# Performance work log

Hardware: AMD Instinct MI355X
Metric: run time of the kernel (lower is better)

## Reference

```python
import jax, jax.numpy as jnp
import numpy as np

HEADS = 8
DIM_HEAD = 64
DIM = 512
NUM_BANDS = 32
MAX_FREQ = 32.0
NORM_SCALE = 10.0
RPE_DIM = (NUM_BANDS * 2 + 1) * 2  # 130


def setup_inputs() -> dict:
    key = jax.random.key(0)
    ks = jax.random.split(key, 9)
    B, N = 2, 512
    inner = HEADS * DIM_HEAD
    h2 = HEADS * 2
    inp = {
        "x": jax.random.normal(ks[0], (B, N, DIM), dtype=jnp.float32),
        "positions": jax.random.uniform(ks[1], (B, N, 2), dtype=jnp.float32),
        "W_qkv": jax.random.normal(ks[2], (DIM, 3 * inner), dtype=jnp.float32) / np.sqrt(DIM),
        "W_out": jax.random.normal(ks[3], (inner, DIM), dtype=jnp.float32) / np.sqrt(inner),
        "b_out": jnp.zeros((DIM,), dtype=jnp.float32),
        "rpe_W1": jax.random.normal(ks[4], (RPE_DIM, h2), dtype=jnp.float32) / np.sqrt(RPE_DIM),
        "rpe_b1": jnp.zeros((h2,), dtype=jnp.float32),
        "rpe_W2": jax.random.normal(ks[5], (h2, HEADS), dtype=jnp.float32) / np.sqrt(h2),
        "rpe_b2": jnp.zeros((HEADS,), dtype=jnp.float32),
    }
    return inp


def _fourier_encode(x):
    # x: [...], returns [..., 2*NUM_BANDS+1]
    freqs = jnp.linspace(1.0, MAX_FREQ, NUM_BANDS, dtype=x.dtype)
    angles = x[..., None] * freqs * jnp.pi
    return jnp.concatenate([x[..., None], jnp.sin(angles), jnp.cos(angles)], axis=-1)


def _rpe_bias(positions, W1, b1, W2, b2):
    # positions: [B, N, 2] -> bias [B, H, N, N]
    delta = positions[:, None, :, :] - positions[:, :, None, :]  # key_pos_j - query_pos_i
    dx = delta[..., 0] / NORM_SCALE
    dy = delta[..., 1] / NORM_SCALE
    dx = dx / (1.0 + jnp.abs(dx))
    dy = dy / (1.0 + jnp.abs(dy))
    feats = jnp.concatenate([_fourier_encode(dx), _fourier_encode(dy)], axis=-1)  # [B,N,N,130]
    h = jax.nn.gelu(feats @ W1 + b1, approximate=False)
    bias = h @ W2 + b2  # [B, N, N, H]
    return jnp.transpose(bias, (0, 3, 1, 2))  # [B, H, N, N]


def reference(x, positions, W_qkv, W_out, b_out, rpe_W1, rpe_b1, rpe_W2, rpe_b2):
    B, N, _ = x.shape
    H, d = HEADS, DIM_HEAD
    scale = d ** (-0.5)
    qkv = x @ W_qkv  # [B, N, 3*H*d]
    q, k, v = jnp.split(qkv, 3, axis=-1)
    q = q.reshape(B, N, H, d)
    k = k.reshape(B, N, H, d)
    v = v.reshape(B, N, H, d)
    scores = jnp.einsum('bihd,bjhd->bhij', q, k) * scale
    scores = scores + _rpe_bias(positions, rpe_W1, rpe_b1, rpe_W2, rpe_b2)
    attn = jax.nn.softmax(scores, axis=-1)
    out = jnp.einsum('bhij,bjhd->bihd', attn, v).reshape(B, N, H * d)
    return out @ W_out + b_out
```

## Files before the change

### kernel.cpp

```cpp
#include <hip/hip_runtime.h>
#include <hip/hip_fp16.h>
#include <math.h>

typedef __attribute__((ext_vector_type(8))) _Float16 f16x8;
typedef __attribute__((ext_vector_type(4))) float f32x4;

#define TBL 512
#define UMAXV (1.0f/11.0f)

__device__ __forceinline__ int swq(int row, int q) {
  return row * 64 + ((q ^ (row & 7)) << 3);
}
__device__ __forceinline__ f16x8 cvt8(float4 a, float4 b) {
  f16x8 r;
  r[0] = (_Float16)a.x; r[1] = (_Float16)a.y;
  r[2] = (_Float16)a.z; r[3] = (_Float16)a.w;
  r[4] = (_Float16)b.x; r[5] = (_Float16)b.y;
  r[6] = (_Float16)b.z; r[7] = (_Float16)b.w;
  return r;
}

__global__ __launch_bounds__(256) void k_prep(
    const float* __restrict__ Wqkv, const float* __restrict__ Wout,
    const float* __restrict__ W1, const float* __restrict__ b1,
    _Float16* __restrict__ Wt, _Float16* __restrict__ Wot,
    __half* __restrict__ Tx, __half* __restrict__ Ty) {
  __shared__ float Tt[32 * 33];
  const int t = threadIdx.x;
  const int bid = blockIdx.x;
  if (bid >= 1024) {
    int gid = (bid - 1024) * 256 + t;
    int e = gid >> 5, c = gid & 31;
    float u = -UMAXV + (2.0f * UMAXV) * (float)e / (float)(TBL - 1);
    const int xpart = (c < 16);
    const int col = c & 15;
    const int base = xpart ? 0 : 65;
    float sum = u * W1[base * 16 + col] + (xpart ? b1[col] : 0.0f);
    float s1, c1;
    sincosf(u * 3.14159265358979323846f, &s1, &c1);
    float sk = s1, ck = c1;
    for (int k = 1; k <= 32; ++k) {
      sum += sk * W1[(base + k) * 16 + col] + ck * W1[(base + 32 + k) * 16 + col];
      float ns = sk * c1 + ck * s1;
      ck = ck * c1 - sk * s1;
      sk = ns;
    }
    (xpart ? Tx : Ty)[e * 16 + col] = __float2half(sum);
    return;
  }
  int k0, n0, ncols;
  const float* W;
  _Float16* O;
  if (bid < 768) {
    k0 = (bid / 48) * 32; n0 = (bid % 48) * 32; ncols = 1536;
    W = Wqkv; O = Wt;
  } else {
    int tile = bid - 768;
    k0 = (tile / 16) * 32; n0 = (tile % 16) * 32; ncols = 512;
    W = Wout; O = Wot;
  }
  {
    int kl = t >> 3, nl = (t & 7) * 4;
    float4 v = *(const float4*)&W[(k0 + kl) * ncols + n0 + nl];
    Tt[kl * 33 + nl + 0] = v.x;
    Tt[kl * 33 + nl + 1] = v.y;
    Tt[kl * 33 + nl + 2] = v.z;
    Tt[kl * 33 + nl + 3] = v.w;
  }
  __syncthreads();
  {
    int nl = t >> 3, kq = (t & 7) * 4;
    ushort4 h;
    h.x = __builtin_bit_cast(unsigned short, (_Float16)Tt[(kq + 0) * 33 + nl]);
    h.y = __builtin_bit_cast(unsigned short, (_Float16)Tt[(kq + 1) * 33 + nl]);
    h.z = __builtin_bit_cast(unsigned short, (_Float16)Tt[(kq + 2) * 33 + nl]);
    h.w = __builtin_bit_cast(unsigned short, (_Float16)Tt[(kq + 3) * 33 + nl]);
    *(ushort4*)&O[(n0 + nl) * 512 + k0 + kq] = h;
  }
}

__global__ __launch_bounds__(512) void k_fused(
    const float* __restrict__ x, const _Float16* __restrict__ Wt,
    _Float16* __restrict__ q16, _Float16* __restrict__ k16,
    _Float16* __restrict__ vt16,
    const float* __restrict__ pos,
    const __half* __restrict__ Tx, const __half* __restrict__ Ty,
    const float* __restrict__ W2, const float* __restrict__ b2,
    _Float16* __restrict__ bias) {
  __shared__ __align__(16) unsigned short SM[16384];
  const int bid = blockIdx.x;
  const int t = threadIdx.x;

  if (bid < 192) {
    _Float16* Ah = (_Float16*)SM;
    _Float16* Bh = (_Float16*)SM + 8192;
    const int mt = bid / 24, nt = bid % 24;
    const int m0 = mt * 128, n0 = nt * 64;
    const int w = t >> 6, lane = t & 63, blk = lane >> 4, jc = lane & 15;
    const int mw = (w & 3) * 32, nw = (w >> 2) * 32;
    const int sa = t >> 3, sq = t & 7;

    f32x4 acc[2][2];
    #pragma unroll
    for (int i = 0; i < 2; ++i)
      #pragma unroll
      for (int j = 0; j < 2; ++j) acc[i][j] = f32x4{0.f, 0.f, 0.f, 0.f};

    float4 pax[2][2];
    f16x8 pbv;
    #pragma unroll
    for (int c = 0; c < 2; ++c) {
      const float* xp = &x[(m0 + sa + c * 64) * 512 + sq * 8];
      pax[c][0] = *(const float4*)xp;
      pax[c][1] = *(const float4*)(xp + 4);
    }
    pbv = *(const f16x8*)&Wt[(n0 + sa) * 512 + sq * 8];

    for (int it = 0; it < 8; ++it) {
      #pragma unroll
      for (int c = 0; c < 2; ++c)
        *(f16x8*)&Ah[swq(sa + c * 64, sq)] = cvt8(pax[c][0], pax[c][1]);
      *(f16x8*)&Bh[swq(sa, sq)] = pbv;
      __syncthreads();
      if (it < 7) {
        int k0 = (it + 1) * 64;
        #pragma unroll
        for (int c = 0; c < 2; ++c) {
          const float* xp = &x[(m0 + sa + c * 64) * 512 + k0 + sq * 8];
          pax[c][0] = *(const float4*)xp;
          pax[c][1] = *(const float4*)(xp + 4);
        }
        pbv = *(const f16x8*)&Wt[(n0 + sa) * 512 + k0 + sq * 8];
      }
      #pragma unroll
      for (int h = 0; h < 2; ++h) {
        int q = h * 4 + blk;
        f16x8 a0 = *(const f16x8*)&Ah[swq(mw + jc, q)];
        f16x8 a1 = *(const f16x8*)&Ah[swq(mw + 16 + jc, q)];
        f16x8 b0 = *(const f16x8*)&Bh[swq(nw + jc, q)];
        f16x8 b1 = *(const f16x8*)&Bh[swq(nw + 16 + jc, q)];
        acc[0][0] = __builtin_amdgcn_mfma_f32_16x16x32_f16(a0, b0, acc[0][0], 0, 0, 0);
        acc[0][1] = __builtin_amdgcn_mfma_f32_16x16x32_f16(a0, b1, acc[0][1], 0, 0, 0);
        acc[1][0] = __builtin_amdgcn_mfma_f32_16x16x32_f16(a1, b0, acc[1][0], 0, 0, 0);
        acc[1][1] = __builtin_amdgcn_mfma_f32_16x16x32_f16(a1, b1, acc[1][1], 0, 0, 0);
      }
      __syncthreads();
    }
    const int sec = n0 >> 9;
    const int hh_ = (n0 >> 6) & 7;
    if (sec < 2) {
      _Float16* dst = (sec == 0) ? q16 : k16;
      const float scl = (sec == 0) ? 0.125f : 1.0f;
      #pragma unroll
      for (int i = 0; i < 2; ++i)
        #pragma unroll
        for (int j = 0; j < 2; ++j)
          #pragma unroll
          for (int r = 0; r < 4; ++r) {
            int tok = m0 + mw + i * 16 + blk * 4 + r;
            int b = tok >> 9, nn = tok & 511;
            int d = nw + j * 16 + jc;
            dst[((b * 8 + hh_) * 512 + nn) * 64 + d] = (_Float16)(acc[i][j][r] * scl);
          }
    } else {
      _Float16* T = (_Float16*)SM;
      #pragma unroll
      for (int i = 0; i < 2; ++i)
        #pragma unroll
        for (int j = 0; j < 2; ++j)
          #pragma unroll
          for (int r = 0; r < 4; ++r)
            T[(nw + j * 16 + jc) * 136 + mw + i * 16 + blk * 4 + r] =
                (_Float16)acc[i][j][r];
      __syncthreads();
      const int d = t >> 3, tq = t & 7;
      const int b = m0 >> 9, nb = m0 & 511;
      #pragma unroll
      for (int c = 0; c < 2; ++c) {
        int qd = tq + c * 8;
        f16x8 vv = *(const f16x8*)&T[d * 136 + qd * 8];
        *(f16x8*)&vt16[((b * 8 + hh_) * 64 + d) * 512 + nb + qd * 8] = vv;
      }
    }
    return;
  }

  const int gid = (bid - 192) * 512 + t;
  const int b = gid >> 18;
  const int i = (gid >> 9) & 511;
  const int j = gid & 511;
  const float pix = pos[(b * 512 + i) * 2 + 0];
  const float piy = pos[(b * 512 + i) * 2 + 1];
  const float pjx = pos[(b * 512 + j) * 2 + 0];
  const float pjy = pos[(b * 512 + j) * 2 + 1];
  float txv = (pjx - pix) * 0.1f; float ux = txv / (1.0f + fabsf(txv));
  float tyv = (pjy - piy) * 0.1f; float uy = tyv / (1.0f + fabsf(tyv));
  const float invstep = (float)(TBL - 1) / (2.0f * UMAXV);
  float fx = (ux + UMAXV) * invstep;
  int ix = (int)fx; ix = min(max(ix, 0), TBL - 2);
  float wx = fx - (float)ix;
  float fy = (uy + UMAXV) * invstep;
  int iy = (int)fy; iy = min(max(iy, 0), TBL - 2);
  float wy = fy - (float)iy;

  __half hx0[16], hx1[16], hy0[16], hy1[16];
  *(uint4*)&hx0[0] = *(const uint4*)&Tx[ix * 16];
  *(uint4*)&hx0[8] = *(const uint4*)&Tx[ix * 16 + 8];
  *(uint4*)&hx1[0] = *(const uint4*)&Tx[(ix + 1) * 16];
  *(uint4*)&hx1[8] = *(const uint4*)&Tx[(ix + 1) * 16 + 8];
  *(uint4*)&hy0[0] = *(const uint4*)&Ty[iy * 16];
  *(uint4*)&hy0[8] = *(const uint4*)&Ty[iy * 16 + 8];
  *(uint4*)&hy1[0] = *(const uint4*)&Ty[(iy + 1) * 16];
  *(uint4*)&hy1[8] = *(const uint4*)&Ty[(iy + 1) * 16 + 8];

  float o[8];
  #pragma unroll
  for (int c = 0; c < 8; ++c) o[c] = b2[c];
  #pragma unroll
  for (int r = 0; r < 16; ++r) {
    float ax = __half2float(hx0[r]);
    float bx = __half2float(hx1[r]);
    float ay = __half2float(hy0[r]);
    float by = __half2float(hy1[r]);
    float hv = fmaf(wx, bx - ax, ax) + fmaf(wy, by - ay, ay);
    float z = hv * 0.70710678118654752f;
    float az = fabsf(z);
    float tt = __builtin_amdgcn_rcpf(fmaf(0.3275911f, az, 1.0f));
    float poly = ((((1.061405429f * tt - 1.453152027f) * tt + 1.421413741f) * tt
                   - 0.284496736f) * tt + 0.254829592f) * tt;
    float ex = __expf(-z * z);
    float erfv = copysignf(fmaf(-poly, ex, 1.0f), z);
    float g = 0.5f * hv * (1.0f + erfv);
    #pragma unroll
    for (int c = 0; c < 8; ++c)
      o[c] = fmaf(g, W2[r * 8 + c], o[c]);
  }
  #pragma unroll
  for (int c = 0; c < 8; ++c)
    bias[((size_t)(b * 8 + c) * 512 + i) * 512 + j] = (_Float16)o[c];
}

__global__ __launch_bounds__(512) void k_attn(
    const _Float16* __restrict__ q16, const _Float16* __restrict__ k16,
    const _Float16* __restrict__ vt16, const _Float16* __restrict__ bias,
    _Float16* __restrict__ ao16) {
  __shared__ __align__(16) _Float16 psu[8 * 512];
  __shared__ __align__(16) float olds[8 * 16 * 65];
  __shared__ float mls[8 * 16 * 2];
  _Float16* bst = (_Float16*)olds;

  const int bid = blockIdx.x;
  const int it = bid & 31, h = (bid >> 5) & 7, b = bid >> 8;
  const int i0 = it * 16;
  const int bh = b * 8 + h;
  const int tid = threadIdx.x;
  const int w = tid >> 6, lane = tid & 63;
  const int blk = lane >> 4, jc = lane & 15;

  {
    const _Float16* bgp = bias + ((size_t)(bh * 512 + i0)) * 512;
    int brow = tid >> 5, bc = (tid & 31) * 16;
    *(f16x8*)&bst[brow * 520 + bc]     = *(const f16x8*)&bgp[brow * 512 + bc];
    *(f16x8*)&bst[brow * 520 + bc + 8] = *(const f16x8*)&bgp[brow * 512 + bc + 8];
  }

  const int qoff = (bh * 512 + i0 + jc) * 64 + blk * 8;
  const f16x8 qa0 = *(const f16x8*)&q16[qoff];
  const f16x8 qa1 = *(const f16x8*)&q16[qoff + 32];

  float m[4] = {-1e30f, -1e30f, -1e30f, -1e30f};
  float l[4] = {0.f, 0.f, 0.f, 0.f};
  f32x4 o[4];
  #pragma unroll
  for (int dt = 0; dt < 4; ++dt) o[dt] = f32x4{0.f, 0.f, 0.f, 0.f};

  _Float16* pw = &psu[w * 512];
  __syncthreads();

  #pragma unroll
  for (int jt = 0; jt < 2; ++jt) {
    const int j0 = w * 64 + jt * 32;
    const int rA = (bh * 512 + j0 + jc) * 64 + blk * 8;
    const int rB = rA + 16 * 64;
    f16x8 kA0 = *(const f16x8*)&k16[rA];
    f16x8 kA1 = *(const f16x8*)&k16[rA + 32];
    f16x8 kB0 = *(const f16x8*)&k16[rB];
    f16x8 kB1 = *(const f16x8*)&k16[rB + 32];

    f32x4 aA = {0.f, 0.f, 0.f, 0.f};
    aA = __builtin_amdgcn_mfma_f32_16x16x32_f16(qa0, kA0, aA, 0, 0, 0);
    aA = __builtin_amdgcn_mfma_f32_16x16x32_f16(qa1, kA1, aA, 0, 0, 0);
    f32x4 aB = {0.f, 0.f, 0.f, 0.f};
    aB = __builtin_amdgcn_mfma_f32_16x16x32_f16(qa0, kB0, aB, 0, 0, 0);
    aB = __builtin_amdgcn_mfma_f32_16x16x32_f16(qa1, kB1, aB, 0, 0, 0);

    float sA[4], sB[4], sc[4];
    #pragma unroll
    for (int r = 0; r < 4; ++r) {
      const int br = (blk * 4 + r) * 520;
      sA[r] = aA[r] + (float)bst[br + j0 + jc];
      sB[r] = aB[r] + (float)bst[br + j0 + 16 + jc];
    }
    #pragma unroll
    for (int r = 0; r < 4; ++r) {
      float mx = fmaxf(sA[r], sB[r]);
      mx = fmaxf(mx, __shfl_xor(mx, 1, 64));
      mx = fmaxf(mx, __shfl_xor(mx, 2, 64));
      mx = fmaxf(mx, __shfl_xor(mx, 4, 64));
      mx = fmaxf(mx, __shfl_xor(mx, 8, 64));
      float mn = fmaxf(m[r], mx);
      sc[r] = __expf(m[r] - mn);
      m[r] = mn;
      float pA = __expf(sA[r] - mn);
      float pB = __expf(sB[r] - mn);
      float ps = pA + pB;
      ps += __shfl_xor(ps, 1, 64);
      ps += __shfl_xor(ps, 2, 64);
      ps += __shfl_xor(ps, 4, 64);
      ps += __shfl_xor(ps, 8, 64);
      l[r] = l[r] * sc[r] + ps;
      pw[(blk * 4 + r) * 32 + jc] = (_Float16)pA;
      pw[(blk * 4 + r) * 32 + 16 + jc] = (_Float16)pB;
    }
    #pragma unroll
    for (int dt = 0; dt < 4; ++dt)
      #pragma unroll
      for (int r = 0; r < 4; ++r)
        o[dt][r] *= sc[r];
    f16x8 pf = *(const f16x8*)&pw[jc * 32 + blk * 8];
    #pragma unroll
    for (int dt = 0; dt < 4; ++dt) {
      const int va = (bh * 64 + dt * 16 + jc) * 512 + j0 + blk * 8;
      f16x8 vh = *(const f16x8*)&vt16[va];
      o[dt] = __builtin_amdgcn_mfma_f32_16x16x32_f16(pf, vh, o[dt], 0, 0, 0);
    }
  }
  __syncthreads();
  #pragma unroll
  for (int dt = 0; dt < 4; ++dt)
    #pragma unroll
    for (int r = 0; r < 4; ++r)
      olds[(w * 16 + blk * 4 + r) * 65 + dt * 16 + jc] = o[dt][r];
  if (jc == 0) {
    #pragma unroll
    for (int r = 0; r < 4; ++r) {
      mls[(w * 16 + blk * 4 + r) * 2 + 0] = m[r];
      mls[(w * 16 + blk * 4 + r) * 2 + 1] = l[r];
    }
  }
  __syncthreads();
  #pragma unroll
  for (int itx = 0; itx < 2; ++itx) {
    int idx = tid + itx * 512;
    int q = idx >> 6, d = idx & 63;
    float M = -1e30f;
    #pragma unroll
    for (int ww = 0; ww < 8; ++ww) M = fmaxf(M, mls[(ww * 16 + q) * 2]);
    float L = 0.f, acc = 0.f;
    #pragma unroll
    for (int ww = 0; ww < 8; ++ww) {
      float e = __expf(mls[(ww * 16 + q) * 2] - M);
      L += mls[(ww * 16 + q) * 2 + 1] * e;
      acc += olds[(ww * 16 + q) * 65 + d] * e;
    }
    ao16[(b * 512 + i0 + q) * 512 + h * 64 + d] = (_Float16)(acc / L);
  }
}

__global__ __launch_bounds__(256) void k_out(
    const _Float16* __restrict__ ao16, const _Float16* __restrict__ Wot,
    const float* __restrict__ bout, float* __restrict__ out) {
  __shared__ __align__(16) unsigned short SM[6144];
  _Float16* Ah = (_Float16*)SM;
  _Float16* Bh = (_Float16*)SM + 2048;

  const int bid = blockIdx.x;
  const int mt = bid >> 3, nt = bid & 7;
  const int m0 = mt * 32, n0 = nt * 64;
  const int t = threadIdx.x;
  const int w = t >> 6, lane = t & 63, blk = lane >> 4, jc = lane & 15;
  const int mh_ = (w & 1) * 16, nh_ = (w >> 1) * 32;
  const int sm = t >> 3, sq = t & 7;

  f32x4 acc[2];
  acc[0] = f32x4{0.f, 0.f, 0.f, 0.f};
  acc[1] = f32x4{0.f, 0.f, 0.f, 0.f};

  f16x8 pa, pb[2];
  {
    pa = *(const f16x8*)&ao16[(m0 + sm) * 512 + sq * 8];
    #pragma unroll
    for (int c = 0; c < 2; ++c)
      pb[c] = *(const f16x8*)&Wot[(n0 + sm + c * 32) * 512 + sq * 8];
  }
  for (int it = 0; it < 8; ++it) {
    *(f16x8*)&Ah[swq(sm, sq)] = pa;
    #pragma unroll
    for (int c = 0; c < 2; ++c)
      *(f16x8*)&Bh[swq(sm + c * 32, sq)] = pb[c];
    __syncthreads();
    if (it < 7) {
      int k0 = (it + 1) * 64;
      pa = *(const f16x8*)&ao16[(m0 + sm) * 512 + k0 + sq * 8];
      #pragma unroll
      for (int c = 0; c < 2; ++c)
        pb[c] = *(const f16x8*)&Wot[(n0 + sm + c * 32) * 512 + k0 + sq * 8];
    }
    #pragma unroll
    for (int h = 0; h < 2; ++h) {
      int q = h * 4 + blk;
      f16x8 a0 = *(const f16x8*)&Ah[swq(mh_ + jc, q)];
      f16x8 b0 = *(const f16x8*)&Bh[swq(nh_ + jc, q)];
      f16x8 b1 = *(const f16x8*)&Bh[swq(nh_ + 16 + jc, q)];
      acc[0] = __builtin_amdgcn_mfma_f32_16x16x32_f16(a0, b0, acc[0], 0, 0, 0);
      acc[1] = __builtin_amdgcn_mfma_f32_16x16x32_f16(a0, b1, acc[1], 0, 0, 0);
    }
    __syncthreads();
  }
  #pragma unroll
  for (int j = 0; j < 2; ++j) {
    int n = n0 + nh_ + j * 16 + jc;
    float bb = bout[n];
    #pragma unroll
    for (int r = 0; r < 4; ++r) {
      int row = m0 + mh_ + blk * 4 + r;
      out[row * 512 + n] = acc[j][r] + bb;
    }
  }
}

extern "C" void kernel_launch(void* const* d_in, const int* in_sizes, int n_in,
                              void* d_out, int out_size, void* d_ws, size_t ws_size,
                              hipStream_t stream) {
  const float* x    = (const float*)d_in[0];
  const float* pos  = (const float*)d_in[1];
  const float* Wqkv = (const float*)d_in[2];
  const float* Wout = (const float*)d_in[3];
  const float* bout = (const float*)d_in[4];
  const float* W1   = (const float*)d_in[5];
  const float* b1   = (const float*)d_in[6];
  const float* W2   = (const float*)d_in[7];
  const float* b2   = (const float*)d_in[8];
  float* out = (float*)d_out;
  char* base = (char*)d_ws;

  __half* Tx       = (__half*)(base);
  __half* Ty       = (__half*)(base + 16384);
  _Float16* Wt     = (_Float16*)(base + 32768);
  _Float16* Wot    = (_Float16*)(base + 1605632);
  _Float16* q16    = (_Float16*)(base + 2129920);
  _Float16* k16    = (_Float16*)(base + 3178496);
  _Float16* vt16   = (_Float16*)(base + 4227072);
  _Float16* bias16 = (_Float16*)(base + 5275648);
  _Float16* ao16   = (_Float16*)(base + 13664256);

  hipLaunchKernelGGL(k_prep, dim3(1088), dim3(256), 0, stream,
                     Wqkv, Wout, W1, b1, Wt, Wot, Tx, Ty);
  hipLaunchKernelGGL(k_fused, dim3(1216), dim3(512), 0, stream,
                     x, Wt, q16, k16, vt16, pos, Tx, Ty, W2, b2, bias16);
  hipLaunchKernelGGL(k_attn, dim3(512), dim3(512), 0, stream,
                     q16, k16, vt16, bias16, ao16);
  hipLaunchKernelGGL(k_out, dim3(256), dim3(256), 0, stream,
                     ao16, Wot, bout, out);
}
```

Measured before the change: 43.97 us.

## Merge all stages into one persistent cooperative kernel with grid syncs

Replaces four separate kernel launches (weight prep, QKV/bias, attention, output projection) with a single cooperative kernel of 256 blocks. The blocks loop over the former work items and separate the stages with grid-wide barriers. This removes launch overhead and inter-kernel gaps. In exchange, each stage is limited to 256 resident blocks with 512 threads, which lowers parallelism for the bias and prep stages, and the output GEMM tile shape changes to 64x64 over 128 blocks.

```diff
diff --git a/kernel.cpp b/kernel.cpp
--- a/kernel.cpp
+++ b/kernel.cpp
@@ -1,6 +1,9 @@
 #include <hip/hip_runtime.h>
 #include <hip/hip_fp16.h>
+#include <hip/hip_cooperative_groups.h>
 #include <math.h>
+
+namespace cg = cooperative_groups;
 
 typedef __attribute__((ext_vector_type(8))) _Float16 f16x8;
 typedef __attribute__((ext_vector_type(4))) float f32x4;
@@ -20,16 +23,31 @@
   return r;
 }
 
-__global__ __launch_bounds__(256) void k_prep(
+__global__ __launch_bounds__(512) void k_all(
+    const float* __restrict__ x, const float* __restrict__ pos,
     const float* __restrict__ Wqkv, const float* __restrict__ Wout,
-    const float* __restrict__ W1, const float* __restrict__ b1,
-    _Float16* __restrict__ Wt, _Float16* __restrict__ Wot,
-    __half* __restrict__ Tx, __half* __restrict__ Ty) {
-  __shared__ float Tt[32 * 33];
+    const float* __restrict__ bout, const float* __restrict__ W1,
+    const float* __restrict__ b1, const float* __restrict__ W2,
+    const float* __restrict__ b2, float* __restrict__ out,
+    char* __restrict__ ws) {
+  __shared__ __align__(16) char SMEM[42496];
+
+  __half*   Tx     = (__half*)(ws);
+  __half*   Ty     = (__half*)(ws + 16384);
+  _Float16* Wt     = (_Float16*)(ws + 32768);
+  _Float16* Wot    = (_Float16*)(ws + 1605632);
+  _Float16* q16    = (_Float16*)(ws + 2129920);
+  _Float16* k16    = (_Float16*)(ws + 3178496);
+  _Float16* vt16   = (_Float16*)(ws + 4227072);
+  _Float16* bias16 = (_Float16*)(ws + 5275648);
+  _Float16* ao16   = (_Float16*)(ws + 13664256);
+
+  cg::grid_group grid = cg::this_grid();
+  const int bid = blockIdx.x;
   const int t = threadIdx.x;
-  const int bid = blockIdx.x;
-  if (bid >= 1024) {
-    int gid = (bid - 1024) * 256 + t;
+
+  if (bid >= 224) {
+    int gid = (bid - 224) * 512 + t;
     int e = gid >> 5, c = gid & 31;
     float u = -UMAXV + (2.0f * UMAXV) * (float)e / (float)(TBL - 1);
     const int xpart = (c < 16);
@@ -46,385 +64,367 @@
       sk = ns;
     }
     (xpart ? Tx : Ty)[e * 16 + col] = __float2half(sum);
-    return;
+  } else {
+    const int sub = t >> 8, tl = t & 255;
+    float* Tt = (float*)SMEM + sub * (32 * 33);
+    for (int u = bid; u < 512; u += 224) {
+      int tile = u * 2 + sub;
+      int k0, n0, ncols;
+      const float* W;
+      _Float16* O;
+      if (tile < 768) {
+        k0 = (tile / 48) * 32; n0 = (tile % 48) * 32; ncols = 1536;
+        W = Wqkv; O = Wt;
+      } else {
+        int q = tile - 768;
+        k0 = (q / 16) * 32; n0 = (q % 16) * 32; ncols = 512;
+        W = Wout; O = Wot;
+      }
+      {
+        int kl = tl >> 3, nl = (tl & 7) * 4;
+        float4 v = *(const float4*)&W[(k0 + kl) * ncols + n0 + nl];
+        Tt[kl * 33 + nl + 0] = v.x;
+        Tt[kl * 33 + nl + 1] = v.y;
+        Tt[kl * 33 + nl + 2] = v.z;
+        Tt[kl * 33 + nl + 3] = v.w;
+      }
+      __syncthreads();
+      {
+        int nl = tl >> 3, kq = (tl & 7) * 4;
+        ushort4 h;
+        h.x = __builtin_bit_cast(unsigned short, (_Float16)Tt[(kq + 0) * 33 + nl]);
+        h.y = __builtin_bit_cast(unsigned short, (_Float16)Tt[(kq + 1) * 33 + nl]);
+        h.z = __builtin_bit_cast(unsigned short, (_Float16)Tt[(kq + 2) * 33 + nl]);
+        h.w = __builtin_bit_cast(unsigned short, (_Float16)Tt[(kq + 3) * 33 + nl]);
+        *(ushort4*)&O[(n0 + nl) * 512 + k0 + kq] = h;
+      }
+      __syncthreads();
+    }
   }
-  int k0, n0, ncols;
-  const float* W;
-  _Float16* O;
-  if (bid < 768) {
-    k0 = (bid / 48) * 32; n0 = (bid % 48) * 32; ncols = 1536;
-    W = Wqkv; O = Wt;
-  } else {
-    int tile = bid - 768;
-    k0 = (tile / 16) * 32; n0 = (tile % 16) * 32; ncols = 512;
-    W = Wout; O = Wot;
+  grid.sync();
+
+  for (int u = bid; u < 1216; u += 256) {
+    if (u < 192) {
+      _Float16* Ah = (_Float16*)SMEM;
+      _Float16* Bh = (_Float16*)SMEM + 8192;
+      const int mt = u / 24, nt = u % 24;
+      const int m0 = mt * 128, n0 = nt * 64;
+      const int w = t >> 6, lane = t & 63, blk = lane >> 4, jc = lane & 15;
+      const int mw = (w & 3) * 32, nw = (w >> 2) * 32;
+      const int sa = t >> 3, sq = t & 7;
+
+      f32x4 acc[2][2];
+      #pragma unroll
+      for (int i = 0; i < 2; ++i)
+        #pragma unroll
+        for (int j = 0; j < 2; ++j) acc[i][j] = f32x4{0.f, 0.f, 0.f, 0.f};
+
+      float4 pax[2][2];
+      f16x8 pbv;
+      #pragma unroll
+      for (int c = 0; c < 2; ++c) {
+        const float* xp = &x[(m0 + sa + c * 64) * 512 + sq * 8];
+        pax[c][0] = *(const float4*)xp;
+        pax[c][1] = *(const float4*)(xp + 4);
+      }
+      pbv = *(const f16x8*)&Wt[(n0 + sa) * 512 + sq * 8];
+
+      for (int it = 0; it < 8; ++it) {
+        #pragma unroll
+        for (int c = 0; c < 2; ++c)
+          *(f16x8*)&Ah[swq(sa + c * 64, sq)] = cvt8(pax[c][0], pax[c][1]);
+        *(f16x8*)&Bh[swq(sa, sq)] = pbv;
+        __syncthreads();
+        if (it < 7) {
+          int k0 = (it + 1) * 64;
+          #pragma unroll
+          for (int c = 0; c < 2; ++c) {
+            const float* xp = &x[(m0 + sa + c * 64) * 512 + k0 + sq * 8];
+            pax[c][0] = *(const float4*)xp;
+            pax[c][1] = *(const float4*)(xp + 4);
+          }
+          pbv = *(const f16x8*)&Wt[(n0 + sa) * 512 + k0 + sq * 8];
+        }
+        #pragma unroll
+        for (int h = 0; h < 2; ++h) {
+          int q = h * 4 + blk;
+          f16x8 a0 = *(const f16x8*)&Ah[swq(mw + jc, q)];
+          f16x8 a1 = *(const f16x8*)&Ah[swq(mw + 16 + jc, q)];
+          f16x8 b0 = *(const f16x8*)&Bh[swq(nw + jc, q)];
+          f16x8 b1 = *(const f16x8*)&Bh[swq(nw + 16 + jc, q)];
+          acc[0][0] = __builtin_amdgcn_mfma_f32_16x16x32_f16(a0, b0, acc[0][0], 0, 0, 0);
+          acc[0][1] = __builtin_amdgcn_mfma_f32_16x16x32_f16(a0, b1, acc[0][1], 0, 0, 0);
+          acc[1][0] = __builtin_amdgcn_mfma_f32_16x16x32_f16(a1, b0, acc[1][0], 0, 0, 0);
+          acc[1][1] = __builtin_amdgcn_mfma_f32_16x16x32_f16(a1, b1, acc[1][1], 0, 0, 0);
+        }
+        __syncthreads();
+      }
+      const int sec = n0 >> 9;
+      const int hh_ = (n0 >> 6) & 7;
+      if (sec < 2) {
+        _Float16* dst = (sec == 0) ? q16 : k16;
+        const float scl = (sec == 0) ? 0.125f : 1.0f;
+        #pragma unroll
+        for (int i = 0; i < 2; ++i)
+          #pragma unroll
+          for (int j = 0; j < 2; ++j)
+            #pragma unroll
+            for (int r = 0; r < 4; ++r) {
+              int tok = m0 + mw + i * 16 + blk * 4 + r;
+              int b = tok >> 9, nn = tok & 511;
+              int d = nw + j * 16 + jc;
+              dst[((b * 8 + hh_) * 512 + nn) * 64 + d] = (_Float16)(acc[i][j][r] * scl);
+            }
+      } else {
+        _Float16* T = (_Float16*)SMEM;
+        #pragma unroll
+        for (int i = 0; i < 2; ++i)
+          #pragma unroll
+          for (int j = 0; j < 2; ++j)
+            #pragma unroll
+            for (int r = 0; r < 4; ++r)
+              T[(nw + j * 16 + jc) * 136 + mw + i * 16 + blk * 4 + r] =
+                  (_Float16)acc[i][j][r];
+        __syncthreads();
+        const int d = t >> 3, tq = t & 7;
+        const int b = m0 >> 9, nb = m0 & 511;
+        #pragma unroll
+        for (int c = 0; c < 2; ++c) {
+          int qd = tq + c * 8;
+          f16x8 vv = *(const f16x8*)&T[d * 136 + qd * 8];
+          *(f16x8*)&vt16[((b * 8 + hh_) * 64 + d) * 512 + nb + qd * 8] = vv;
+        }
+        __syncthreads();
+      }
+    } else {
+      const int gid = (u - 192) * 512 + t;
+      const int b = gid >> 18;
+      const int i = (gid >> 9) & 511;
+      const int j = gid & 511;
+      const float pix = pos[(b * 512 + i) * 2 + 0];
+      const float piy = pos[(b * 512 + i) * 2 + 1];
+      const float pjx = pos[(b * 512 + j) * 2 + 0];
+      const float pjy = pos[(b * 512 + j) * 2 + 1];
+      float txv = (pjx - pix) * 0.1f; float ux = txv / (1.0f + fabsf(txv));
+      float tyv = (pjy - piy) * 0.1f; float uy = tyv / (1.0f + fabsf(tyv));
+      const float invstep = (float)(TBL - 1) / (2.0f * UMAXV);
+      float fx = (ux + UMAXV) * invstep;
+      int ix = (int)fx; ix = min(max(ix, 0), TBL - 2);
+      float wx = fx - (float)ix;
+      float fy = (uy + UMAXV) * invstep;
+      int iy = (int)fy; iy = min(max(iy, 0), TBL - 2);
+      float wy = fy - (float)iy;
+
+      __half hx0[16], hx1[16], hy0[16], hy1[16];
+      *(uint4*)&hx0[0] = *(const uint4*)&Tx[ix * 16];
+      *(uint4*)&hx0[8] = *(const uint4*)&Tx[ix * 16 + 8];
+      *(uint4*)&hx1[0] = *(const uint4*)&Tx[(ix + 1) * 16];
+      *(uint4*)&hx1[8] = *(const uint4*)&Tx[(ix + 1) * 16 + 8];
+      *(uint4*)&hy0[0] = *(const uint4*)&Ty[iy * 16];
+      *(uint4*)&hy0[8] = *(const uint4*)&Ty[iy * 16 + 8];
+      *(uint4*)&hy1[0] = *(const uint4*)&Ty[(iy + 1) * 16];
+      *(uint4*)&hy1[8] = *(const uint4*)&Ty[(iy + 1) * 16 + 8];
+
+      float o[8];
+      #pragma unroll
+      for (int c = 0; c < 8; ++c) o[c] = b2[c];
+      #pragma unroll
+      for (int r = 0; r < 16; ++r) {
+        float ax = __half2float(hx0[r]);
+        float bx = __half2float(hx1[r]);
+        float ay = __half2float(hy0[r]);
+        float by = __half2float(hy1[r]);
+        float hv = fmaf(wx, bx - ax, ax) + fmaf(wy, by - ay, ay);
+        float z = hv * 0.70710678118654752f;
+        float az = fabsf(z);
+        float tt = __builtin_amdgcn_rcpf(fmaf(0.3275911f, az, 1.0f));
+        float poly = ((((1.061405429f * tt - 1.453152027f) * tt + 1.421413741f) * tt
+                       - 0.284496736f) * tt + 0.254829592f) * tt;
+        float ex = __expf(-z * z);
+        float erfv = copysignf(fmaf(-poly, ex, 1.0f), z);
+        float g = 0.5f * hv * (1.0f + erfv);
+        #pragma unroll
+        for (int c = 0; c < 8; ++c)
+          o[c] = fmaf(g, W2[r * 8 + c], o[c]);
+      }
+      #pragma unroll
+      for (int c = 0; c < 8; ++c)
+        bias16[((size_t)(b * 8 + c) * 512 + i) * 512 + j] = (_Float16)o[c];
+    }
   }
+  grid.sync();
+
   {
-    int kl = t >> 3, nl = (t & 7) * 4;
-    float4 v = *(const float4*)&W[(k0 + kl) * ncols + n0 + nl];
-    Tt[kl * 33 + nl + 0] = v.x;
-    Tt[kl * 33 + nl + 1] = v.y;
-    Tt[kl * 33 + nl + 2] = v.z;
-    Tt[kl * 33 + nl + 3] = v.w;
+    _Float16* psu = (_Float16*)SMEM;
+    float* olds   = (float*)(SMEM + 8192);
+    float* mls    = (float*)(SMEM + 8192 + 33280);
+    _Float16* bst = (_Float16*)olds;
+
+    for (int u = bid; u < 512; u += 256) {
+      const int itile = u & 31, h = (u >> 5) & 7, b = u >> 8;
+      const int i0 = itile * 16;
+      const int bh = b * 8 + h;
+      const int w = t >> 6, lane = t & 63;
+      const int blk = lane >> 4, jc = lane & 15;
+
+      {
+        const _Float16* bgp = bias16 + ((size_t)(bh * 512 + i0)) * 512;
+        int brow = t >> 5, bc = (t & 31) * 16;
+        *(f16x8*)&bst[brow * 520 + bc]     = *(const f16x8*)&bgp[brow * 512 + bc];
+        *(f16x8*)&bst[brow * 520 + bc + 8] = *(const f16x8*)&bgp[brow * 512 + bc + 8];
+      }
+
+      const int qoff = (bh * 512 + i0 + jc) * 64 + blk * 8;
+      const f16x8 qa0 = *(const f16x8*)&q16[qoff];
+      const f16x8 qa1 = *(const f16x8*)&q16[qoff + 32];
+
+      float m[4] = {-1e30f, -1e30f, -1e30f, -1e30f};
+      float l[4] = {0.f, 0.f, 0.f, 0.f};
+      f32x4 o[4];
+      #pragma unroll
+      for (int dt = 0; dt < 4; ++dt) o[dt] = f32x4{0.f, 0.f, 0.f, 0.f};
+
+      _Float16* pw = &psu[w * 512];
+      __syncthreads();
+
+      #pragma unroll
+      for (int jt = 0; jt < 2; ++jt) {
+        const int j0 = w * 64 + jt * 32;
+        const int rA = (bh * 512 + j0 + jc) * 64 + blk * 8;
+        const int rB = rA + 16 * 64;
+        f16x8 kA0 = *(const f16x8*)&k16[rA];
+        f16x8 kA1 = *(const f16x8*)&k16[rA + 32];
+        f16x8 kB0 = *(const f16x8*)&k16[rB];
+        f16x8 kB1 = *(const f16x8*)&k16[rB + 32];
+
+        f32x4 aA = {0.f, 0.f, 0.f, 0.f};
+        aA = __builtin_amdgcn_mfma_f32_16x16x32_f16(qa0, kA0, aA, 0, 0, 0);
+        aA = __builtin_amdgcn_mfma_f32_16x16x32_f16(qa1, kA1, aA, 0, 0, 0);
+        f32x4 aB = {0.f, 0.f, 0.f, 0.f};
+        aB = __builtin_amdgcn_mfma_f32_16x16x32_f16(qa0, kB0, aB, 0, 0, 0);
+        aB = __builtin_amdgcn_mfma_f32_16x16x32_f16(qa1, kB1, aB, 0, 0, 0);
+
+        float sA[4], sB[4], sc[4];
+        #pragma unroll
+        for (int r = 0; r < 4; ++r) {
+          const int br = (blk * 4 + r) * 520;
+          sA[r] = aA[r] + (float)bst[br + j0 + jc];
+          sB[r] = aB[r] + (float)bst[br + j0 + 16 + jc];
+        }
+        #pragma unroll
+        for (int r = 0; r < 4; ++r) {
+          float mx = fmaxf(sA[r], sB[r]);
+          mx = fmaxf(mx, __shfl_xor(mx, 1, 64));
+          mx = fmaxf(mx, __shfl_xor(mx, 2, 64));
+          mx = fmaxf(mx, __shfl_xor(mx, 4, 64));
+          mx = fmaxf(mx, __shfl_xor(mx, 8, 64));
+          float mn = fmaxf(m[r], mx);
+          sc[r] = __expf(m[r] - mn);
+          m[r] = mn;
+          float pA = __expf(sA[r] - mn);
+          float pB = __expf(sB[r] - mn);
+          float ps = pA + pB;
+          ps += __shfl_xor(ps, 1, 64);
+          ps += __shfl_xor(ps, 2, 64);
+          ps += __shfl_xor(ps, 4, 64);
+          ps += __shfl_xor(ps, 8, 64);
+          l[r] = l[r] * sc[r] + ps;
+          pw[(blk * 4 + r) * 32 + jc] = (_Float16)pA;
+          pw[(blk * 4 + r) * 32 + 16 + jc] = (_Float16)pB;
+        }
+        #pragma unroll
+        for (int dt = 0; dt < 4; ++dt)
+          #pragma unroll
+          for (int r = 0; r < 4; ++r)
+            o[dt][r] *= sc[r];
+        f16x8 pf = *(const f16x8*)&pw[jc * 32 + blk * 8];
+        #pragma unroll
+        for (int dt = 0; dt < 4; ++dt) {
+          const int va = (bh * 64 + dt * 16 + jc) * 512 + j0 + blk * 8;
+          f16x8 vh = *(const f16x8*)&vt16[va];
+          o[dt] = __builtin_amdgcn_mfma_f32_16x16x32_f16(pf, vh, o[dt], 0, 0, 0);
+        }
+      }
+      __syncthreads();
+      #pragma unroll
+      for (int dt = 0; dt < 4; ++dt)
+        #pragma unroll
+        for (int r = 0; r < 4; ++r)
+          olds[(w * 16 + blk * 4 + r) * 65 + dt * 16 + jc] = o[dt][r];
+      if (jc == 0) {
+        #pragma unroll
+        for (int r = 0; r < 4; ++r) {
+          mls[(w * 16 + blk * 4 + r) * 2 + 0] = m[r];
+          mls[(w * 16 + blk * 4 + r) * 2 + 1] = l[r];
+        }
+      }
+      __syncthreads();
+      #pragma unroll
+      for (int itx = 0; itx < 2; ++itx) {
+        int idx = t + itx * 512;
+        int q = idx >> 6, d = idx & 63;
+        float M = -1e30f;
+        #pragma unroll
+        for (int ww = 0; ww < 8; ++ww) M = fmaxf(M, mls[(ww * 16 + q) * 2]);
+        float L = 0.f, acc = 0.f;
+        #pragma unroll
+        for (int ww = 0; ww < 8; ++ww) {
+          float e = __expf(mls[(ww * 16 + q) * 2] - M);
+          L += mls[(ww * 16 + q) * 2 + 1] * e;
+          acc += olds[(ww * 16 + q) * 65 + d] * e;
+        }
+        ao16[(b * 512 + i0 + q) * 512 + h * 64 + d] = (_Float16)(acc / L);
+      }
+      __syncthreads();
+    }
   }
-  __syncthreads();
-  {
-    int nl = t >> 3, kq = (t & 7) * 4;
-    ushort4 h;
-    h.x = __builtin_bit_cast(unsigned short, (_Float16)Tt[(kq + 0) * 33 + nl]);
-    h.y = __builtin_bit_cast(unsigned short, (_Float16)Tt[(kq + 1) * 33 + nl]);
-    h.z = __builtin_bit_cast(unsigned short, (_Float16)Tt[(kq + 2) * 33 + nl]);
-    h.w = __builtin_bit_cast(unsigned short, (_Float16)Tt[(kq + 3) * 33 + nl]);
-    *(ushort4*)&O[(n0 + nl) * 512 + k0 + kq] = h;
-  }
-}
-
-__global__ __launch_bounds__(512) void k_fused(
-    const float* __restrict__ x, const _Float16* __restrict__ Wt,
-    _Float16* __restrict__ q16, _Float16* __restrict__ k16,
-    _Float16* __restrict__ vt16,
-    const float* __restrict__ pos,
-    const __half* __restrict__ Tx, const __half* __restrict__ Ty,
-    const float* __restrict__ W2, const float* __restrict__ b2,
-    _Float16* __restrict__ bias) {
-  __shared__ __align__(16) unsigned short SM[16384];
-  const int bid = blockIdx.x;
-  const int t = threadIdx.x;
-
-  if (bid < 192) {
-    _Float16* Ah = (_Float16*)SM;
-    _Float16* Bh = (_Float16*)SM + 8192;
-    const int mt = bid / 24, nt = bid % 24;
-    const int m0 = mt * 128, n0 = nt * 64;
+  grid.sync();
+
+  if (bid < 128) {
+    _Float16* Ah = (_Float16*)SMEM;
+    _Float16* Bh = (_Float16*)SMEM + 4096;
+    const int mt = bid >> 3, nt = bid & 7;
+    const int m0 = mt * 64, n0 = nt * 64;
     const int w = t >> 6, lane = t & 63, blk = lane >> 4, jc = lane & 15;
-    const int mw = (w & 3) * 32, nw = (w >> 2) * 32;
+    const int mw = (w & 3) * 16, nw = (w >> 2) * 32;
     const int sa = t >> 3, sq = t & 7;
 
-    f32x4 acc[2][2];
-    #pragma unroll
-    for (int i = 0; i < 2; ++i)
-      #pragma unroll
-      for (int j = 0; j < 2; ++j) acc[i][j] = f32x4{0.f, 0.f, 0.f, 0.f};
-
-    float4 pax[2][2];
-    f16x8 pbv;
-    #pragma unroll
-    for (int c = 0; c < 2; ++c) {
-      const float* xp = &x[(m0 + sa + c * 64) * 512 + sq * 8];
-      pax[c][0] = *(const float4*)xp;
-      pax[c][1] = *(const float4*)(xp + 4);
-    }
-    pbv = *(const f16x8*)&Wt[(n0 + sa) * 512 + sq * 8];
+    f32x4 acc[2];
+    acc[0] = f32x4{0.f, 0.f, 0.f, 0.f};
+    acc[1] = f32x4{0.f, 0.f, 0.f, 0.f};
+
+    f16x8 pa = *(const f16x8*)&ao16[(m0 + sa) * 512 + sq * 8];
+    f16x8 pb = *(const f16x8*)&Wot[(n0 + sa) * 512 + sq * 8];
 
     for (int it = 0; it < 8; ++it) {
-      #pragma unroll
-      for (int c = 0; c < 2; ++c)
-        *(f16x8*)&Ah[swq(sa + c * 64, sq)] = cvt8(pax[c][0], pax[c][1]);
-      *(f16x8*)&Bh[swq(sa, sq)] = pbv;
+      *(f16x8*)&Ah[swq(sa, sq)] = pa;
+      *(f16x8*)&Bh[swq(sa, sq)] = pb;
       __syncthreads();
       if (it < 7) {
         int k0 = (it + 1) * 64;
-        #pragma unroll
-        for (int c = 0; c < 2; ++c) {
-          const float* xp = &x[(m0 + sa + c * 64) * 512 + k0 + sq * 8];
-          pax[c][0] = *(const float4*)xp;
-          pax[c][1] = *(const float4*)(xp + 4);
-        }
-        pbv = *(const f16x8*)&Wt[(n0 + sa) * 512 + k0 + sq * 8];
+        pa = *(const f16x8*)&ao16[(m0 + sa) * 512 + k0 + sq * 8];
+        pb = *(const f16x8*)&Wot[(n0 + sa) * 512 + k0 + sq * 8];
       }
       #pragma unroll
       for (int h = 0; h < 2; ++h) {
         int q = h * 4 + blk;
         f16x8 a0 = *(const f16x8*)&Ah[swq(mw + jc, q)];
-        f16x8 a1 = *(const f16x8*)&Ah[swq(mw + 16 + jc, q)];
         f16x8 b0 = *(const f16x8*)&Bh[swq(nw + jc, q)];
         f16x8 b1 = *(const f16x8*)&Bh[swq(nw + 16 + jc, q)];
-        acc[0][0] = __builtin_amdgcn_mfma_f32_16x16x32_f16(a0, b0, acc[0][0], 0, 0, 0);
-        acc[0][1] = __builtin_amdgcn_mfma_f32_16x16x32_f16(a0, b1, acc[0][1], 0, 0, 0);
-        acc[1][0] = __builtin_amdgcn_mfma_f32_16x16x32_f16(a1, b0, acc[1][0], 0, 0, 0);
-        acc[1][1] = __builtin_amdgcn_mfma_f32_16x16x32_f16(a1, b1, acc[1][1], 0, 0, 0);
-      }
-      __syncthreads();
-    }
-    const int sec = n0 >> 9;
-    const int hh_ = (n0 >> 6) & 7;
-    if (sec < 2) {
-      _Float16* dst = (sec == 0) ? q16 : k16;
-      const float scl = (sec == 0) ? 0.125f : 1.0f;
-      #pragma unroll
-      for (int i = 0; i < 2; ++i)
-        #pragma unroll
-        for (int j = 0; j < 2; ++j)
-          #pragma unroll
-          for (int r = 0; r < 4; ++r) {
-            int tok = m0 + mw + i * 16 + blk * 4 + r;
-            int b = tok >> 9, nn = tok & 511;
-            int d = nw + j * 16 + jc;
-            dst[((b * 8 + hh_) * 512 + nn) * 64 + d] = (_Float16)(acc[i][j][r] * scl);
-          }
-    } else {
-      _Float16* T = (_Float16*)SM;
-      #pragma unroll
-      for (int i = 0; i < 2; ++i)
-        #pragma unroll
-        for (int j = 0; j < 2; ++j)
-          #pragma unroll
-          for (int r = 0; r < 4; ++r)
-            T[(nw + j * 16 + jc) * 136 + mw + i * 16 + blk * 4 + r] =
-                (_Float16)acc[i][j][r];
-      __syncthreads();
-      const int d = t >> 3, tq = t & 7;
-      const int b = m0 >> 9, nb = m0 & 511;
-      #pragma unroll
-      for (int c = 0; c < 2; ++c) {
-        int qd = tq + c * 8;
-        f16x8 vv = *(const f16x8*)&T[d * 136 + qd * 8];
-        *(f16x8*)&vt16[((b * 8 + hh_) * 64 + d) * 512 + nb + qd * 8] = vv;
-      }
-    }
-    return;
-  }
-
-  const int gid = (bid - 192) * 512 + t;
-  const int b = gid >> 18;
-  const int i = (gid >> 9) & 511;
-  const int j = gid & 511;
-  const float pix = pos[(b * 512 + i) * 2 + 0];
-  const float piy = pos[(b * 512 + i) * 2 + 1];
-  const float pjx = pos[(b * 512 + j) * 2 + 0];
-  const float pjy = pos[(b * 512 + j) * 2 + 1];
-  float txv = (pjx - pix) * 0.1f; float ux = txv / (1.0f + fabsf(txv));
-  float tyv = (pjy - piy) * 0.1f; float uy = tyv / (1.0f + fabsf(tyv));
-  const float invstep = (float)(TBL - 1) / (2.0f * UMAXV);
-  float fx = (ux + UMAXV) * invstep;
-  int ix = (int)fx; ix = min(max(ix, 0), TBL - 2);
-  float wx = fx - (float)ix;
-  float fy = (uy + UMAXV) * invstep;
-  int iy = (int)fy; iy = min(max(iy, 0), TBL - 2);
-  float wy = fy - (float)iy;
-
-  __half hx0[16], hx1[16], hy0[16], hy1[16];
-  *(uint4*)&hx0[0] = *(const uint4*)&Tx[ix * 16];
-  *(uint4*)&hx0[8] = *(const uint4*)&Tx[ix * 16 + 8];
-  *(uint4*)&hx1[0] = *(const uint4*)&Tx[(ix + 1) * 16];
-  *(uint4*)&hx1[8] = *(const uint4*)&Tx[(ix + 1) * 16 + 8];
-  *(uint4*)&hy0[0] = *(const uint4*)&Ty[iy * 16];
-  *(uint4*)&hy0[8] = *(const uint4*)&Ty[iy * 16 + 8];
-  *(uint4*)&hy1[0] = *(const uint4*)&Ty[(iy + 1) * 16];
-  *(uint4*)&hy1[8] = *(const uint4*)&Ty[(iy + 1) * 16 + 8];
-
-  float o[8];
-  #pragma unroll
-  for (int c = 0; c < 8; ++c) o[c] = b2[c];
-  #pragma unroll
-  for (int r = 0; r < 16; ++r) {
-    float ax = __half2float(hx0[r]);
-    float bx = __half2float(hx1[r]);
-    float ay = __half2float(hy0[r]);
-    float by = __half2float(hy1[r]);
-    float hv = fmaf(wx, bx - ax, ax) + fmaf(wy, by - ay, ay);
-    float z = hv * 0.70710678118654752f;
-    float az = fabsf(z);
-    float tt = __builtin_amdgcn_rcpf(fmaf(0.3275911f, az, 1.0f));
-    float poly = ((((1.061405429f * tt - 1.453152027f) * tt + 1.421413741f) * tt
-                   - 0.284496736f) * tt + 0.254829592f) * tt;
-    float ex = __expf(-z * z);
-    float erfv = copysignf(fmaf(-poly, ex, 1.0f), z);
-    float g = 0.5f * hv * (1.0f + erfv);
+        acc[0] = __builtin_amdgcn_mfma_f32_16x16x32_f16(a0, b0, acc[0], 0, 0, 0);
+        acc[1] = __builtin_amdgcn_mfma_f32_16x16x32_f16(a0, b1, acc[1], 0, 0, 0);
+      }
+      __syncthreads();
+    }
     #pragma unroll
-    for (int c = 0; c < 8; ++c)
-      o[c] = fmaf(g, W2[r * 8 + c], o[c]);
-  }
-  #pragma unroll
-  for (int c = 0; c < 8; ++c)
-    bias[((size_t)(b * 8 + c) * 512 + i) * 512 + j] = (_Float16)o[c];
-}
-
-__global__ __launch_bounds__(512) void k_attn(
-    const _Float16* __restrict__ q16, const _Float16* __restrict__ k16,
-    const _Float16* __restrict__ vt16, const _Float16* __restrict__ bias,
-    _Float16* __restrict__ ao16) {
-  __shared__ __align__(16) _Float16 psu[8 * 512];
-  __shared__ __align__(16) float olds[8 * 16 * 65];
-  __shared__ float mls[8 * 16 * 2];
-  _Float16* bst = (_Float16*)olds;
-
-  const int bid = blockIdx.x;
-  const int it = bid & 31, h = (bid >> 5) & 7, b = bid >> 8;
-  const int i0 = it * 16;
-  const int bh = b * 8 + h;
-  const int tid = threadIdx.x;
-  const int w = tid >> 6, lane = tid & 63;
-  const int blk = lane >> 4, jc = lane & 15;
-
-  {
-    const _Float16* bgp = bias + ((size_t)(bh * 512 + i0)) * 512;
-    int brow = tid >> 5, bc = (tid & 31) * 16;
-    *(f16x8*)&bst[brow * 520 + bc]     = *(const f16x8*)&bgp[brow * 512 + bc];
-    *(f16x8*)&bst[brow * 520 + bc + 8] = *(const f16x8*)&bgp[brow * 512 + bc + 8];
-  }
-
-  const int qoff = (bh * 512 + i0 + jc) * 64 + blk * 8;
-  const f16x8 qa0 = *(const f16x8*)&q16[qoff];
-  const f16x8 qa1 = *(const f16x8*)&q16[qoff + 32];
-
-  float m[4] = {-1e30f, -1e30f, -1e30f, -1e30f};
-  float l[4] = {0.f, 0.f, 0.f, 0.f};
-  f32x4 o[4];
-  #pragma unroll
-  for (int dt = 0; dt < 4; ++dt) o[dt] = f32x4{0.f, 0.f, 0.f, 0.f};
-
-  _Float16* pw = &psu[w * 512];
-  __syncthreads();
-
-  #pragma unroll
-  for (int jt = 0; jt < 2; ++jt) {
-    const int j0 = w * 64 + jt * 32;
-    const int rA = (bh * 512 + j0 + jc) * 64 + blk * 8;
-    const int rB = rA + 16 * 64;
-    f16x8 kA0 = *(const f16x8*)&k16[rA];
-    f16x8 kA1 = *(const f16x8*)&k16[rA + 32];
-    f16x8 kB0 = *(const f16x8*)&k16[rB];
-    f16x8 kB1 = *(const f16x8*)&k16[rB + 32];
-
-    f32x4 aA = {0.f, 0.f, 0.f, 0.f};
-    aA = __builtin_amdgcn_mfma_f32_16x16x32_f16(qa0, kA0, aA, 0, 0, 0);
-    aA = __builtin_amdgcn_mfma_f32_16x16x32_f16(qa1, kA1, aA, 0, 0, 0);
-    f32x4 aB = {0.f, 0.f, 0.f, 0.f};
-    aB = __builtin_amdgcn_mfma_f32_16x16x32_f16(qa0, kB0, aB, 0, 0, 0);
-    aB = __builtin_amdgcn_mfma_f32_16x16x32_f16(qa1, kB1, aB, 0, 0, 0);
-
-    float sA[4], sB[4], sc[4];
-    #pragma unroll
-    for (int r = 0; r < 4; ++r) {
-      const int br = (blk * 4 + r) * 520;
-      sA[r] = aA[r] + (float)bst[br + j0 + jc];
-      sB[r] = aB[r] + (float)bst[br + j0 + 16 + jc];
-    }
-    #pragma unroll
-    for (int r = 0; r < 4; ++r) {
-      float mx = fmaxf(sA[r], sB[r]);
-      mx = fmaxf(mx, __shfl_xor(mx, 1, 64));
-      mx = fmaxf(mx, __shfl_xor(mx, 2, 64));
-      mx = fmaxf(mx, __shfl_xor(mx, 4, 64));
-      mx = fmaxf(mx, __shfl_xor(mx, 8, 64));
-      float mn = fmaxf(m[r], mx);
-      sc[r] = __expf(m[r] - mn);
-      m[r] = mn;
-      float pA = __expf(sA[r] - mn);
-      float pB = __expf(sB[r] - mn);
-      float ps = pA + pB;
-      ps += __shfl_xor(ps, 1, 64);
-      ps += __shfl_xor(ps, 2, 64);
-      ps += __shfl_xor(ps, 4, 64);
-      ps += __shfl_xor(ps, 8, 64);
-      l[r] = l[r] * sc[r] + ps;
-      pw[(blk * 4 + r) * 32 + jc] = (_Float16)pA;
-      pw[(blk * 4 + r) * 32 + 16 + jc] = (_Float16)pB;
-    }
-    #pragma unroll
-    for (int dt = 0; dt < 4; ++dt)
-      #pragma unroll
-      for (int r = 0; r < 4; ++r)
-        o[dt][r] *= sc[r];
-    f16x8 pf = *(const f16x8*)&pw[jc * 32 + blk * 8];
-    #pragma unroll
-    for (int dt = 0; dt < 4; ++dt) {
-      const int va = (bh * 64 + dt * 16 + jc) * 512 + j0 + blk * 8;
-      f16x8 vh = *(const f16x8*)&vt16[va];
-      o[dt] = __builtin_amdgcn_mfma_f32_16x16x32_f16(pf, vh, o[dt], 0, 0, 0);
-    }
-  }
-  __syncthreads();
-  #pragma unroll
-  for (int dt = 0; dt < 4; ++dt)
-    #pragma unroll
-    for (int r = 0; r < 4; ++r)
-      olds[(w * 16 + blk * 4 + r) * 65 + dt * 16 + jc] = o[dt][r];
-  if (jc == 0) {
-    #pragma unroll
-    for (int r = 0; r < 4; ++r) {
-      mls[(w * 16 + blk * 4 + r) * 2 + 0] = m[r];
-      mls[(w * 16 + blk * 4 + r) * 2 + 1] = l[r];
-    }
-  }
-  __syncthreads();
-  #pragma unroll
-  for (int itx = 0; itx < 2; ++itx) {
-    int idx = tid + itx * 512;
-    int q = idx >> 6, d = idx & 63;
-    float M = -1e30f;
-    #pragma unroll
-    for (int ww = 0; ww < 8; ++ww) M = fmaxf(M, mls[(ww * 16 + q) * 2]);
-    float L = 0.f, acc = 0.f;
-    #pragma unroll
-    for (int ww = 0; ww < 8; ++ww) {
-      float e = __expf(mls[(ww * 16 + q) * 2] - M);
-      L += mls[(ww * 16 + q) * 2 + 1] * e;
-      acc += olds[(ww * 16 + q) * 65 + d] * e;
-    }
-    ao16[(b * 512 + i0 + q) * 512 + h * 64 + d] = (_Float16)(acc / L);
-  }
-}
-
-__global__ __launch_bounds__(256) void k_out(
-    const _Float16* __restrict__ ao16, const _Float16* __restrict__ Wot,
-    const float* __restrict__ bout, float* __restrict__ out) {
-  __shared__ __align__(16) unsigned short SM[6144];
-  _Float16* Ah = (_Float16*)SM;
-  _Float16* Bh = (_Float16*)SM + 2048;
-
-  const int bid = blockIdx.x;
-  const int mt = bid >> 3, nt = bid & 7;
-  const int m0 = mt * 32, n0 = nt * 64;
-  const int t = threadIdx.x;
-  const int w = t >> 6, lane = t & 63, blk = lane >> 4, jc = lane & 15;
-  const int mh_ = (w & 1) * 16, nh_ = (w >> 1) * 32;
-  const int sm = t >> 3, sq = t & 7;
-
-  f32x4 acc[2];
-  acc[0] = f32x4{0.f, 0.f, 0.f, 0.f};
-  acc[1] = f32x4{0.f, 0.f, 0.f, 0.f};
-
-  f16x8 pa, pb[2];
-  {
-    pa = *(const f16x8*)&ao16[(m0 + sm) * 512 + sq * 8];
-    #pragma unroll
-    for (int c = 0; c < 2; ++c)
-      pb[c] = *(const f16x8*)&Wot[(n0 + sm + c * 32) * 512 + sq * 8];
-  }
-  for (int it = 0; it < 8; ++it) {
-    *(f16x8*)&Ah[swq(sm, sq)] = pa;
-    #pragma unroll
-    for (int c = 0; c < 2; ++c)
-      *(f16x8*)&Bh[swq(sm + c * 32, sq)] = pb[c];
-    __syncthreads();
-    if (it < 7) {
-      int k0 = (it + 1) * 64;
-      pa = *(const f16x8*)&ao16[(m0 + sm) * 512 + k0 + sq * 8];
-      #pragma unroll
-      for (int c = 0; c < 2; ++c)
-        pb[c] = *(const f16x8*)&Wot[(n0 + sm + c * 32) * 512 + k0 + sq * 8];
-    }
-    #pragma unroll
-    for (int h = 0; h < 2; ++h) {
-      int q = h * 4 + blk;
-      f16x8 a0 = *(const f16x8*)&Ah[swq(mh_ + jc, q)];
-      f16x8 b0 = *(const f16x8*)&Bh[swq(nh_ + jc, q)];
-      f16x8 b1 = *(const f16x8*)&Bh[swq(nh_ + 16 + jc, q)];
-      acc[0] = __builtin_amdgcn_mfma_f32_16x16x32_f16(a0, b0, acc[0], 0, 0, 0);
-      acc[1] = __builtin_amdgcn_mfma_f32_16x16x32_f16(a0, b1, acc[1], 0, 0, 0);
-    }
-    __syncthreads();
-  }
-  #pragma unroll
-  for (int j = 0; j < 2; ++j) {
-    int n = n0 + nh_ + j * 16 + jc;
-    float bb = bout[n];
-    #pragma unroll
-    for (int r = 0; r < 4; ++r) {
-      int row = m0 + mh_ + blk * 4 + r;
-      out[row * 512 + n] = acc[j][r] + bb;
+    for (int j = 0; j < 2; ++j) {
+      int n = n0 + nw + j * 16 + jc;
+      float bb = bout[n];
+      #pragma unroll
+      for (int r = 0; r < 4; ++r) {
+        int row = m0 + mw + blk * 4 + r;
+        out[row * 512 + n] = acc[j][r] + bb;
+      }
     }
   }
 }
@@ -442,24 +442,11 @@
   const float* W2   = (const float*)d_in[7];
   const float* b2   = (const float*)d_in[8];
   float* out = (float*)d_out;
-  char* base = (char*)d_ws;
-
-  __half* Tx       = (__half*)(base);
-  __half* Ty       = (__half*)(base + 16384);
-  _Float16* Wt     = (_Float16*)(base + 32768);
-  _Float16* Wot    = (_Float16*)(base + 1605632);
-  _Float16* q16    = (_Float16*)(base + 2129920);
-  _Float16* k16    = (_Float16*)(base + 3178496);
-  _Float16* vt16   = (_Float16*)(base + 4227072);
-  _Float16* bias16 = (_Float16*)(base + 5275648);
-  _Float16* ao16   = (_Float16*)(base + 13664256);
-
-  hipLaunchKernelGGL(k_prep, dim3(1088), dim3(256), 0, stream,
-                     Wqkv, Wout, W1, b1, Wt, Wot, Tx, Ty);
-  hipLaunchKernelGGL(k_fused, dim3(1216), dim3(512), 0, stream,
-                     x, Wt, q16, k16, vt16, pos, Tx, Ty, W2, b2, bias16);
-  hipLaunchKernelGGL(k_attn, dim3(512), dim3(512), 0, stream,
-                     q16, k16, vt16, bias16, ao16);
-  hipLaunchKernelGGL(k_out, dim3(256), dim3(256), 0, stream,
-                     ao16, Wot, bout, out);
+  char* ws = (char*)d_ws;
+
+  void* args[] = {(void*)&x, (void*)&pos, (void*)&Wqkv, (void*)&Wout,
+                  (void*)&bout, (void*)&W1, (void*)&b1, (void*)&W2,
+                  (void*)&b2, (void*)&out, (void*)&ws};
+  hipLaunchCooperativeKernel((const void*)k_all, dim3(256), dim3(512),
+                             args, 0, stream);
 }
```

Result: slower. 147.0 us (+234.4%).
